# Kernel tuning notes

Measured on AMD Instinct MI355X. Metric: run time of the kernel, lower is better.

The kernel has to match this reference:

```python
import jax, jax.numpy as jnp
import numpy as np

H = 1024  # hidden_dim
DT = 0.1
LN_EPS = 1e-5


def setup_inputs() -> dict:
    key = jax.random.key(0)
    ks = jax.random.split(key, 8)
    h = H
    ph = h // 2
    x = jax.random.normal(ks[0], (8, 2048, h), dtype=jnp.float32)
    # S initialized to identity in torch; add small noise so math is non-trivial
    S = jnp.eye(h, dtype=jnp.float32) + 0.02 * jax.random.normal(ks[1], (h, h), dtype=jnp.float32)
    # Hamiltonian MLP: Linear(h,h) -> tanh -> Linear(h,1)
    lim1 = 1.0 / np.sqrt(h)
    W1 = jax.random.uniform(ks[2], (h, h), minval=-lim1, maxval=lim1, dtype=jnp.float32)
    b1 = jax.random.uniform(ks[3], (h,), minval=-lim1, maxval=lim1, dtype=jnp.float32)
    w2 = jax.random.uniform(ks[4], (h,), minval=-lim1, maxval=lim1, dtype=jnp.float32)
    b2 = jax.random.uniform(ks[5], (1,), minval=-lim1, maxval=lim1, dtype=jnp.float32)
    # symplectic structure matrix J (buffer)
    I = jnp.eye(ph, dtype=jnp.float32)
    J = jnp.zeros((h, h), dtype=jnp.float32)
    J = J.at[:ph, ph:].set(I)
    J = J.at[ph:, :ph].set(-I)
    gamma = jnp.ones((h,), dtype=jnp.float32)
    beta = jnp.zeros((h,), dtype=jnp.float32)
    return {"x": x, "S": S, "W1": W1, "b1": b1, "w2": w2, "b2": b2,
            "J": J, "gamma": gamma, "beta": beta, "num_steps": 3}


def reference(x, S, W1, b1, w2, b2, J, gamma, beta, num_steps):
    h = x.shape[-1]
    # Cayley-approx symplectic projection (training branch): S_sym = I + 2*A, A skew part
    A = (S - S.T) * 0.5
    S_sym = jnp.eye(h, dtype=x.dtype) + 2.0 * A
    # z = einsum('ij,...j->...i', S_sym, x)
    z = x @ S_sym.T
    for _ in range(num_steps):
        # analytic grad of H(z) = w2 . tanh(z W1^T + b1) + b2 wrt z
        t = jnp.tanh(z @ W1.T + b1)             # [..., h]
        grad_H = ((1.0 - t * t) * w2) @ W1       # [..., h]
        flow = grad_H @ J.T                      # einsum('ij,...j->...i', J, grad_H)
        z = z + DT * flow
    y = z + x
    # LayerNorm over last dim
    mu = jnp.mean(y, axis=-1, keepdims=True)
    var = jnp.mean((y - mu) ** 2, axis=-1, keepdims=True)
    return (y - mu) * jax.lax.rsqrt(var + LN_EPS) * gamma + beta
```

## Files before the change

kernel.cpp:

```cpp
#include <hip/hip_runtime.h>
#include <hip/hip_bf16.h>

#define H 1024
#define PH 512
#define MROWS 16384
#define DT 0.1f
#define LN_EPS 1e-5f

#define BM 128
#define BN 128
#define BK 64

typedef short s16x8 __attribute__((ext_vector_type(8)));
typedef float f32x4 __attribute__((ext_vector_type(4)));

__device__ __forceinline__ float b2f(short v) {
    union { float f; unsigned u; } c;
    c.u = ((unsigned)(unsigned short)v) << 16;
    return c.f;
}
__device__ __forceinline__ short f2b(float f) {
    union { float f; unsigned u; } c;
    c.f = f;
    unsigned u = c.u;
    unsigned r = u + 0x7FFFu + ((u >> 16) & 1u);
    return (short)(r >> 16);
}
__device__ __forceinline__ float ftanh(float s) {
    float e = __expf(2.0f * s);
    return 1.0f - 2.0f * __builtin_amdgcn_rcpf(e + 1.0f);
}

__global__ __launch_bounds__(256)
void prep_t(const float* __restrict__ S, const float* __restrict__ W1,
            short* __restrict__ Wsym, short* __restrict__ W1b,
            short* __restrict__ Wflow, short* __restrict__ WflowT) {
    __shared__ float T0[64][65];
    __shared__ float T1[64][65];
    __shared__ short Ts[64][66];
    const int I = blockIdx.y * 64, J = blockIdx.x * 64;
    const int c  = threadIdx.x & 63;
    const int r0 = (threadIdx.x >> 6) * 16;
#pragma unroll
    for (int rr = 0; rr < 16; ++rr) {
        int r = r0 + rr;
        T0[r][c] = S[(size_t)(I + r) * H + J + c];
        T1[r][c] = S[(size_t)(J + r) * H + I + c];
    }
    __syncthreads();
    const int pJ = (J + PH) & (H - 1);
    const short sflip = (J >= PH) ? (short)0x8000 : (short)0;
#pragma unroll
    for (int rr = 0; rr < 16; ++rr) {
        int r = r0 + rr;
        size_t rowb = (size_t)(I + r) * H;
        Wsym[rowb + J + c] = f2b(T0[r][c] - T1[c][r]);
        W1b [rowb + J + c] = f2b(W1[rowb + J + c]);
        short wt = (short)(f2b(W1[rowb + pJ + c]) ^ sflip);
        WflowT[rowb + J + c] = wt;
        Ts[r][c] = wt;
    }
    __syncthreads();
#pragma unroll
    for (int rr = 0; rr < 16; ++rr) {
        int r = r0 + rr;
        Wflow[(size_t)(J + r) * H + I + c] = Ts[c][r];
    }
}

__global__ __launch_bounds__(256)
void cvt_x(const float* __restrict__ x, short* __restrict__ xb) {
    int t = blockIdx.x * 256 + threadIdx.x;
    const float4* p = (const float4*)x + (size_t)t * 2;
    float4 f0 = p[0], f1 = p[1];
    s16x8 v;
    v[0] = f2b(f0.x); v[1] = f2b(f0.y); v[2] = f2b(f0.z); v[3] = f2b(f0.w);
    v[4] = f2b(f1.x); v[5] = f2b(f1.y); v[6] = f2b(f1.z); v[7] = f2b(f1.w);
    ((s16x8*)xb)[t] = v;
}

template <int KIND, bool G2D>
__global__ __launch_bounds__(256, 2)
void gemm_k(const short* __restrict__ A, const short* __restrict__ Bw,
            short* __restrict__ out,
            const float* __restrict__ xf,
            const float* __restrict__ w2f,
            const short* __restrict__ u0r,
            const short* __restrict__ pg,
            short* __restrict__ out2,
            float clampv)
{
    __shared__ short As[2][BM * BK];
    __shared__ short Bs[2][BN * BK];

    const int tid  = threadIdx.x;
    const int lane = tid & 63;
    const int wave = tid >> 6;
    const int wm   = wave >> 1;
    const int wn   = wave & 1;

    int m0, n0;
    if (G2D) {
        m0 = blockIdx.y * BM;
        n0 = blockIdx.x * BN;
    } else {
        const int lid   = blockIdx.x;
        const int chunk = ((lid & 7) << 7) | (lid >> 3);
        m0 = (chunk >> 3) * BM;
        n0 = (chunk & 7) * BN;
    }

    const int lrow = lane & 15;
    const int quad = lane >> 4;
    const int swzr = (lrow & 7) << 4;

    const int srow  = lane >> 3;
    const int selem = 8 * ((lane & 7) ^ srow);

    f32x4 acc[4][4] = {};

    auto STAGE = [&](int sel, int k0) {
#pragma unroll
        for (int i = 0; i < 4; ++i) {
            int ch = wave * 4 + i;
            const short* asrc = A  + (size_t)(m0 + ch * 8 + srow) * H + k0 + selem;
            const short* bsrc = Bw + (size_t)(n0 + ch * 8 + srow) * H + k0 + selem;
            __builtin_amdgcn_global_load_lds(
                (const __attribute__((address_space(1))) void*)asrc,
                (__attribute__((address_space(3))) void*)(&As[sel][ch * 512]), 16, 0, 0);
            __builtin_amdgcn_global_load_lds(
                (const __attribute__((address_space(1))) void*)bsrc,
                (__attribute__((address_space(3))) void*)(&Bs[sel][ch * 512]), 16, 0, 0);
        }
    };
    auto COMPUTE = [&](int sel) {
#pragma unroll
        for (int ks = 0; ks < 2; ++ks) {
            s16x8 af[4], bfr[4];
#pragma unroll
            for (int mt = 0; mt < 4; ++mt) {
                int row = wm * 64 + mt * 16 + lrow;
                af[mt] = *(const s16x8*)((const char*)&As[sel][0] + row * 128 +
                                         ((ks * 64 + quad * 16) ^ swzr));
            }
#pragma unroll
            for (int nt = 0; nt < 4; ++nt) {
                int col = wn * 64 + nt * 16 + lrow;
                bfr[nt] = *(const s16x8*)((const char*)&Bs[sel][0] + col * 128 +
                                          ((ks * 64 + quad * 16) ^ swzr));
            }
#pragma unroll
            for (int mt = 0; mt < 4; ++mt)
#pragma unroll
                for (int nt = 0; nt < 4; ++nt)
                    acc[mt][nt] = __builtin_amdgcn_mfma_f32_16x16x32_bf16(
                        bfr[nt], af[mt], acc[mt][nt], 0, 0, 0);
        }
    };

    STAGE(0, 0);
    int cur = 0;
    for (int t = 0; t < (H / BK) - 1; ++t) {
        STAGE(cur ^ 1, (t + 1) * BK);
        asm volatile("s_waitcnt vmcnt(8)" ::: "memory");
        __builtin_amdgcn_s_barrier();
        COMPUTE(cur);
        __builtin_amdgcn_s_barrier();
        cur ^= 1;
    }
    asm volatile("s_waitcnt vmcnt(0)" ::: "memory");
    __builtin_amdgcn_s_barrier();
    COMPUTE(cur);

    float4 bvv[4], wvv[4];
    if (KIND == 1 || KIND == 3 || KIND == 4) {
#pragma unroll
        for (int nt = 0; nt < 4; ++nt) {
            int col = n0 + wn * 64 + nt * 16 + quad * 4;
            bvv[nt] = *(const float4*)(xf + col);
            wvv[nt] = *(const float4*)(w2f + col);
        }
    }
#pragma unroll
    for (int mt = 0; mt < 4; ++mt) {
        const int row = m0 + wm * 64 + mt * 16 + lrow;
        const size_t rbase = (size_t)row * H;
#pragma unroll
        for (int nt = 0; nt < 4; ++nt) {
            const int col = n0 + wn * 64 + nt * 16 + quad * 4;
            const size_t idx = rbase + col;
            f32x4 a = acc[mt][nt];
            short4 o;
            if (KIND == 0) {
                float4 xv = *(const float4*)(xf + idx);
                o.x = f2b(a[0] + xv.x);
                o.y = f2b(a[1] + xv.y);
                o.z = f2b(a[2] + xv.z);
                o.w = f2b(a[3] + xv.w);
                *(short4*)(out + idx) = o;
            } else if (KIND == 1) {
                float t0 = ftanh(a[0] + bvv[nt].x);
                float t1 = ftanh(a[1] + bvv[nt].y);
                float t2 = ftanh(a[2] + bvv[nt].z);
                float t3 = ftanh(a[3] + bvv[nt].w);
                o.x = f2b((1.0f - t0 * t0) * wvv[nt].x);
                o.y = f2b((1.0f - t1 * t1) * wvv[nt].y);
                o.z = f2b((1.0f - t2 * t2) * wvv[nt].z);
                o.w = f2b((1.0f - t3 * t3) * wvv[nt].w);
                *(short4*)(out + idx) = o;
            } else if (KIND == 2) {
                short4 zo = *(const short4*)(out + idx);
                float d0 = fminf(fmaxf(DT * a[0], -clampv), clampv);
                float d1 = fminf(fmaxf(DT * a[1], -clampv), clampv);
                float d2 = fminf(fmaxf(DT * a[2], -clampv), clampv);
                float d3 = fminf(fmaxf(DT * a[3], -clampv), clampv);
                o.x = f2b(b2f(zo.x) + d0);
                o.y = f2b(b2f(zo.y) + d1);
                o.z = f2b(b2f(zo.z) + d2);
                o.w = f2b(b2f(zo.w) + d3);
                *(short4*)(out + idx) = o;
            } else if (KIND == 3) {
                short4 u;
                u.x = f2b(a[0]); u.y = f2b(a[1]); u.z = f2b(a[2]); u.w = f2b(a[3]);
                *(short4*)(out + idx) = u;
                float t0 = ftanh(a[0] + bvv[nt].x);
                float t1 = ftanh(a[1] + bvv[nt].y);
                float t2 = ftanh(a[2] + bvv[nt].z);
                float t3 = ftanh(a[3] + bvv[nt].w);
                o.x = f2b((1.0f - t0 * t0) * wvv[nt].x);
                o.y = f2b((1.0f - t1 * t1) * wvv[nt].y);
                o.z = f2b((1.0f - t2 * t2) * wvv[nt].z);
                o.w = f2b((1.0f - t3 * t3) * wvv[nt].w);
                *(short4*)(out2 + idx) = o;
            } else if (KIND == 4) {
                short4 u4 = *(const short4*)(u0r + idx);
                short4 p4 = *(const short4*)(pg + idx);
                float t0 = ftanh(b2f(u4.x) + a[0] + bvv[nt].x);
                float t1 = ftanh(b2f(u4.y) + a[1] + bvv[nt].y);
                float t2 = ftanh(b2f(u4.z) + a[2] + bvv[nt].z);
                float t3 = ftanh(b2f(u4.w) + a[3] + bvv[nt].w);
                o.x = f2b(b2f(p4.x) + (1.0f - t0 * t0) * wvv[nt].x);
                o.y = f2b(b2f(p4.y) + (1.0f - t1 * t1) * wvv[nt].y);
                o.z = f2b(b2f(p4.z) + (1.0f - t2 * t2) * wvv[nt].z);
                o.w = f2b(b2f(p4.w) + (1.0f - t3 * t3) * wvv[nt].w);
                *(short4*)(out2 + idx) = o;
            } else {
                o.x = f2b(DT * a[0]);
                o.y = f2b(DT * a[1]);
                o.z = f2b(DT * a[2]);
                o.w = f2b(DT * a[3]);
                *(short4*)(out + idx) = o;
            }
        }
    }
}

__global__ __launch_bounds__(256)
void ln_k(const short* __restrict__ z, const float* __restrict__ x,
          const float* __restrict__ gamma, const float* __restrict__ beta,
          float* __restrict__ out) {
    const int row = blockIdx.x;
    const int tid = threadIdx.x;
    const size_t base = (size_t)row * H;
    short4 z4 = ((const short4*)(z + base))[tid];
    float4 x4 = ((const float4*)(x + base))[tid];
    float y0 = b2f(z4.x) + x4.x;
    float y1 = b2f(z4.y) + x4.y;
    float y2 = b2f(z4.z) + x4.z;
    float y3 = b2f(z4.w) + x4.w;
    float s = y0 + y1 + y2 + y3;
    float q = y0 * y0 + y1 * y1 + y2 * y2 + y3 * y3;
#pragma unroll
    for (int off = 32; off > 0; off >>= 1) {
        s += __shfl_down(s, off);
        q += __shfl_down(q, off);
    }
    __shared__ float ss[4], qs[4];
    if ((tid & 63) == 0) { ss[tid >> 6] = s; qs[tid >> 6] = q; }
    __syncthreads();
    s = ss[0] + ss[1] + ss[2] + ss[3];
    q = qs[0] + qs[1] + qs[2] + qs[3];
    const float mu  = s * (1.0f / H);
    const float var = q * (1.0f / H) - mu * mu;
    const float rs  = rsqrtf(var + LN_EPS);
    const int col = tid * 4;
    float4 o;
    o.x = (y0 - mu) * rs * gamma[col + 0] + beta[col + 0];
    o.y = (y1 - mu) * rs * gamma[col + 1] + beta[col + 1];
    o.z = (y2 - mu) * rs * gamma[col + 2] + beta[col + 2];
    o.w = (y3 - mu) * rs * gamma[col + 3] + beta[col + 3];
    ((float4*)(out + base))[tid] = o;
}

extern "C" void kernel_launch(void* const* d_in, const int* in_sizes, int n_in,
                              void* d_out, int out_size, void* d_ws, size_t ws_size,
                              hipStream_t stream) {
    int ix = 0;
    for (int i = 0; i < n_in; ++i)
        if (in_sizes[i] == MROWS * H) { ix = i; break; }

    const float *x, *S, *W1, *b1, *w2, *gamma, *beta;
    if (ix == 0) {
        x     = (const float*)d_in[0];
        S     = (const float*)d_in[1];
        W1    = (const float*)d_in[2];
        b1    = (const float*)d_in[3];
        w2    = (const float*)d_in[4];
        gamma = (const float*)d_in[7];
        beta  = (const float*)d_in[8];
    } else {
        S     = (const float*)d_in[1];
        W1    = (const float*)d_in[2];
        b1    = (const float*)d_in[3];
        beta  = (const float*)d_in[5];
        gamma = (const float*)d_in[6];
        w2    = (const float*)d_in[8];
        x     = (const float*)d_in[ix];
    }

    const size_t MB = 1024 * 1024;
    float* out    = (float*)d_out;
    short* xb     = (short*)d_out;
    short* u0     = (short*)d_out;
    char*  hi     = (char*)d_out + 32 * MB;
    short* Wsym   = (short*)(hi);
    short* W1b    = (short*)(hi + 2 * MB);
    short* Wflow  = (short*)(hi + 4 * MB);
    short* WflowT = (short*)(hi + 6 * MB);
    short* GT     = (short*)(hi + 8 * MB);
    short* z      = (short*)d_ws;
    short* gsumA  = (short*)((char*)d_ws + 32 * MB);
    short* gsumB  = (short*)((char*)d_ws + 64 * MB);

    const bool fast = ws_size >= 96 * MB;

    prep_t<<<dim3(16, 16), 256, 0, stream>>>(S, W1, Wsym, W1b, Wflow, WflowT);
    cvt_x <<<(MROWS * H / 8) / 256, 256, 0, stream>>>(x, xb);

    const int nblk = (H / BN) * (MROWS / BM);
    if (fast) {
        gemm_k<5, true><<<dim3(H / BN, H / BM), 256, 0, stream>>>(
            W1b, WflowT, GT, nullptr, nullptr, nullptr, nullptr, nullptr, 0.0f);
        gemm_k<0, false><<<nblk, 256, 0, stream>>>(
            xb, Wsym, z, x, nullptr, nullptr, nullptr, nullptr, 0.0f);
        gemm_k<3, false><<<nblk, 256, 0, stream>>>(
            z, W1b, u0, b1, w2, nullptr, nullptr, gsumA, 0.0f);
        gemm_k<4, false><<<nblk, 256, 0, stream>>>(
            gsumA, GT, nullptr, b1, w2, u0, gsumA, gsumB, 0.0f);
        gemm_k<4, false><<<nblk, 256, 0, stream>>>(
            gsumB, GT, nullptr, b1, w2, u0, gsumB, gsumA, 0.0f);
        gemm_k<2, false><<<nblk, 256, 0, stream>>>(
            gsumA, Wflow, z, nullptr, nullptr, nullptr, nullptr, nullptr, 0.03f);
    } else {
        short* g = (short*)d_out;
        gemm_k<0, false><<<nblk, 256, 0, stream>>>(
            xb, Wsym, z, x, nullptr, nullptr, nullptr, nullptr, 0.0f);
        for (int step = 0; step < 3; ++step) {
            gemm_k<1, false><<<nblk, 256, 0, stream>>>(
                z, W1b, g, b1, w2, nullptr, nullptr, nullptr, 0.0f);
            gemm_k<2, false><<<nblk, 256, 0, stream>>>(
                g, Wflow, z, nullptr, nullptr, nullptr, nullptr, nullptr, 0.01f);
        }
    }
    ln_k<<<MROWS, 256, 0, stream>>>(z, x, gamma, beta, out);
}
```

Before: 426.6 us.

## Fold symmetric projection into weights, fuse final flow GEMM, single-buffer LDS

Precomputes Wu = W1·(S−Sᵀ)ᵀ-style combined weights so the first hidden GEMM reads bf16 x directly, which removes the separate z = x·S_symᵀ GEMM pass. It merges the final flow GEMM with the x·(S−Sᵀ) product into one GEMM with a doubled K (KIND 7). LayerNorm then adds 2x, which accounts for the identity part of S_sym. The GEMM drops LDS double buffering in favour of a single buffer with __syncthreads and raises the occupancy hint to 4 waves. The single buffer saves LDS for occupancy but loses load/compute overlap, and the reassociation changes bf16 rounding, including the dropped clamp on the fused path.

```diff
diff --git a/kernel.cpp b/kernel.cpp
--- a/kernel.cpp
+++ b/kernel.cpp
@@ -33,8 +33,9 @@
 
 __global__ __launch_bounds__(256)
 void prep_t(const float* __restrict__ S, const float* __restrict__ W1,
-            short* __restrict__ Wsym, short* __restrict__ W1b,
-            short* __restrict__ Wflow, short* __restrict__ WflowT) {
+            short* __restrict__ Wsym, short* __restrict__ WsymT,
+            short* __restrict__ W1b,
+            short* __restrict__ Wfd, short* __restrict__ WflowT) {
     __shared__ float T0[64][65];
     __shared__ float T1[64][65];
     __shared__ short Ts[64][66];
@@ -54,8 +55,10 @@
     for (int rr = 0; rr < 16; ++rr) {
         int r = r0 + rr;
         size_t rowb = (size_t)(I + r) * H;
-        Wsym[rowb + J + c] = f2b(T0[r][c] - T1[c][r]);
-        W1b [rowb + J + c] = f2b(W1[rowb + J + c]);
+        float d = T0[r][c] - T1[c][r];
+        Wsym [rowb + J + c] = f2b(d);
+        WsymT[rowb + J + c] = f2b(-d);
+        W1b  [rowb + J + c] = f2b(W1[rowb + J + c]);
         short wt = (short)(f2b(W1[rowb + pJ + c]) ^ sflip);
         WflowT[rowb + J + c] = wt;
         Ts[r][c] = wt;
@@ -64,7 +67,7 @@
 #pragma unroll
     for (int rr = 0; rr < 16; ++rr) {
         int r = r0 + rr;
-        Wflow[(size_t)(J + r) * H + I + c] = Ts[c][r];
+        Wfd[(size_t)(J + r) * H + I + c] = f2b(DT * b2f(Ts[c][r]));
     }
 }
 
@@ -80,7 +83,7 @@
 }
 
 template <int KIND, bool G2D>
-__global__ __launch_bounds__(256, 2)
+__global__ __launch_bounds__(256, 4)
 void gemm_k(const short* __restrict__ A, const short* __restrict__ Bw,
             short* __restrict__ out,
             const float* __restrict__ xf,
@@ -88,10 +91,12 @@
             const short* __restrict__ u0r,
             const short* __restrict__ pg,
             short* __restrict__ out2,
+            const short* __restrict__ A2,
+            const short* __restrict__ B2,
             float clampv)
 {
-    __shared__ short As[2][BM * BK];
-    __shared__ short Bs[2][BN * BK];
+    __shared__ short As[BM * BK];
+    __shared__ short Bs[BN * BK];
 
     const int tid  = threadIdx.x;
     const int lane = tid & 63;
@@ -119,34 +124,40 @@
 
     f32x4 acc[4][4] = {};
 
-    auto STAGE = [&](int sel, int k0) {
+    const int KSTEPS = (KIND == 7) ? (2 * H / BK) : (H / BK);
+    for (int t = 0; t < KSTEPS; ++t) {
+        const int k0 = t * BK;
+        const short* Au = A;
+        const short* Bu = Bw;
+        if (KIND == 7 && k0 >= H) { Au = A2; Bu = B2; }
+        const int kk = k0 & (H - 1);
 #pragma unroll
         for (int i = 0; i < 4; ++i) {
             int ch = wave * 4 + i;
-            const short* asrc = A  + (size_t)(m0 + ch * 8 + srow) * H + k0 + selem;
-            const short* bsrc = Bw + (size_t)(n0 + ch * 8 + srow) * H + k0 + selem;
+            const short* asrc = Au + (size_t)(m0 + ch * 8 + srow) * H + kk + selem;
+            const short* bsrc = Bu + (size_t)(n0 + ch * 8 + srow) * H + kk + selem;
             __builtin_amdgcn_global_load_lds(
                 (const __attribute__((address_space(1))) void*)asrc,
-                (__attribute__((address_space(3))) void*)(&As[sel][ch * 512]), 16, 0, 0);
+                (__attribute__((address_space(3))) void*)(As + ch * 512), 16, 0, 0);
             __builtin_amdgcn_global_load_lds(
                 (const __attribute__((address_space(1))) void*)bsrc,
-                (__attribute__((address_space(3))) void*)(&Bs[sel][ch * 512]), 16, 0, 0);
-        }
-    };
-    auto COMPUTE = [&](int sel) {
+                (__attribute__((address_space(3))) void*)(Bs + ch * 512), 16, 0, 0);
+        }
+        __syncthreads();
+
 #pragma unroll
         for (int ks = 0; ks < 2; ++ks) {
             s16x8 af[4], bfr[4];
 #pragma unroll
             for (int mt = 0; mt < 4; ++mt) {
                 int row = wm * 64 + mt * 16 + lrow;
-                af[mt] = *(const s16x8*)((const char*)&As[sel][0] + row * 128 +
+                af[mt] = *(const s16x8*)((const char*)As + row * 128 +
                                          ((ks * 64 + quad * 16) ^ swzr));
             }
 #pragma unroll
             for (int nt = 0; nt < 4; ++nt) {
                 int col = wn * 64 + nt * 16 + lrow;
-                bfr[nt] = *(const s16x8*)((const char*)&Bs[sel][0] + col * 128 +
+                bfr[nt] = *(const s16x8*)((const char*)Bs + col * 128 +
                                           ((ks * 64 + quad * 16) ^ swzr));
             }
 #pragma unroll
@@ -156,21 +167,8 @@
                     acc[mt][nt] = __builtin_amdgcn_mfma_f32_16x16x32_bf16(
                         bfr[nt], af[mt], acc[mt][nt], 0, 0, 0);
         }
-    };
-
-    STAGE(0, 0);
-    int cur = 0;
-    for (int t = 0; t < (H / BK) - 1; ++t) {
-        STAGE(cur ^ 1, (t + 1) * BK);
-        asm volatile("s_waitcnt vmcnt(8)" ::: "memory");
-        __builtin_amdgcn_s_barrier();
-        COMPUTE(cur);
-        __builtin_amdgcn_s_barrier();
-        cur ^= 1;
-    }
-    asm volatile("s_waitcnt vmcnt(0)" ::: "memory");
-    __builtin_amdgcn_s_barrier();
-    COMPUTE(cur);
+        __syncthreads();
+    }
 
     float4 bvv[4], wvv[4];
     if (KIND == 1 || KIND == 3 || KIND == 4) {
@@ -210,10 +208,10 @@
                 *(short4*)(out + idx) = o;
             } else if (KIND == 2) {
                 short4 zo = *(const short4*)(out + idx);
-                float d0 = fminf(fmaxf(DT * a[0], -clampv), clampv);
-                float d1 = fminf(fmaxf(DT * a[1], -clampv), clampv);
-                float d2 = fminf(fmaxf(DT * a[2], -clampv), clampv);
-                float d3 = fminf(fmaxf(DT * a[3], -clampv), clampv);
+                float d0 = fminf(fmaxf(a[0], -clampv), clampv);
+                float d1 = fminf(fmaxf(a[1], -clampv), clampv);
+                float d2 = fminf(fmaxf(a[2], -clampv), clampv);
+                float d3 = fminf(fmaxf(a[3], -clampv), clampv);
                 o.x = f2b(b2f(zo.x) + d0);
                 o.y = f2b(b2f(zo.y) + d1);
                 o.z = f2b(b2f(zo.z) + d2);
@@ -244,12 +242,18 @@
                 o.z = f2b(b2f(p4.z) + (1.0f - t2 * t2) * wvv[nt].z);
                 o.w = f2b(b2f(p4.w) + (1.0f - t3 * t3) * wvv[nt].w);
                 *(short4*)(out2 + idx) = o;
-            } else {
+            } else if (KIND == 5) {
                 o.x = f2b(DT * a[0]);
                 o.y = f2b(DT * a[1]);
                 o.z = f2b(DT * a[2]);
                 o.w = f2b(DT * a[3]);
                 *(short4*)(out + idx) = o;
+            } else {
+                o.x = f2b(a[0]);
+                o.y = f2b(a[1]);
+                o.z = f2b(a[2]);
+                o.w = f2b(a[3]);
+                *(short4*)(out + idx) = o;
             }
         }
     }
@@ -258,16 +262,16 @@
 __global__ __launch_bounds__(256)
 void ln_k(const short* __restrict__ z, const float* __restrict__ x,
           const float* __restrict__ gamma, const float* __restrict__ beta,
-          float* __restrict__ out) {
+          float* __restrict__ out, float xmul) {
     const int row = blockIdx.x;
     const int tid = threadIdx.x;
     const size_t base = (size_t)row * H;
     short4 z4 = ((const short4*)(z + base))[tid];
     float4 x4 = ((const float4*)(x + base))[tid];
-    float y0 = b2f(z4.x) + x4.x;
-    float y1 = b2f(z4.y) + x4.y;
-    float y2 = b2f(z4.z) + x4.z;
-    float y3 = b2f(z4.w) + x4.w;
+    float y0 = fmaf(xmul, x4.x, b2f(z4.x));
+    float y1 = fmaf(xmul, x4.y, b2f(z4.y));
+    float y2 = fmaf(xmul, x4.z, b2f(z4.z));
+    float y3 = fmaf(xmul, x4.w, b2f(z4.w));
     float s = y0 + y1 + y2 + y3;
     float q = y0 * y0 + y1 * y1 + y2 * y2 + y3 * y3;
 #pragma unroll
@@ -320,47 +324,62 @@
 
     const size_t MB = 1024 * 1024;
     float* out    = (float*)d_out;
-    short* xb     = (short*)d_out;
     short* u0     = (short*)d_out;
     char*  hi     = (char*)d_out + 32 * MB;
     short* Wsym   = (short*)(hi);
-    short* W1b    = (short*)(hi + 2 * MB);
-    short* Wflow  = (short*)(hi + 4 * MB);
+    short* WsymT  = (short*)(hi + 2 * MB);
+    short* W1b    = (short*)(hi + 4 * MB);
     short* WflowT = (short*)(hi + 6 * MB);
-    short* GT     = (short*)(hi + 8 * MB);
-    short* z      = (short*)d_ws;
+    short* Wfd    = (short*)(hi + 8 * MB);
+    short* Wu     = (short*)(hi + 10 * MB);
+    short* GT     = (short*)(hi + 12 * MB);
+    short* xb     = (short*)d_ws;
     short* gsumA  = (short*)((char*)d_ws + 32 * MB);
     short* gsumB  = (short*)((char*)d_ws + 64 * MB);
+    short* z      = gsumB;
 
     const bool fast = ws_size >= 96 * MB;
-
-    prep_t<<<dim3(16, 16), 256, 0, stream>>>(S, W1, Wsym, W1b, Wflow, WflowT);
-    cvt_x <<<(MROWS * H / 8) / 256, 256, 0, stream>>>(x, xb);
-
-    const int nblk = (H / BN) * (MROWS / BM);
+    const int  nblk = (H / BN) * (MROWS / BM);
+
+    prep_t<<<dim3(16, 16), 256, 0, stream>>>(S, W1, Wsym, WsymT, W1b, Wfd, WflowT);
+
     if (fast) {
+        cvt_x<<<(MROWS * H / 8) / 256, 256, 0, stream>>>(x, xb);
+        gemm_k<0, true><<<dim3(H / BN, H / BM), 256, 0, stream>>>(
+            W1b, WsymT, Wu, W1, nullptr, nullptr, nullptr, nullptr,
+            nullptr, nullptr, 0.0f);
         gemm_k<5, true><<<dim3(H / BN, H / BM), 256, 0, stream>>>(
-            W1b, WflowT, GT, nullptr, nullptr, nullptr, nullptr, nullptr, 0.0f);
+            W1b, WflowT, GT, nullptr, nullptr, nullptr, nullptr, nullptr,
+            nullptr, nullptr, 0.0f);
+        gemm_k<3, false><<<nblk, 256, 0, stream>>>(
+            xb, Wu, u0, b1, w2, nullptr, nullptr, gsumA,
+            nullptr, nullptr, 0.0f);
+        gemm_k<4, false><<<nblk, 256, 0, stream>>>(
+            gsumA, GT, nullptr, b1, w2, u0, gsumA, gsumB,
+            nullptr, nullptr, 0.0f);
+        gemm_k<4, false><<<nblk, 256, 0, stream>>>(
+            gsumB, GT, nullptr, b1, w2, u0, gsumB, gsumA,
+            nullptr, nullptr, 0.0f);
+        gemm_k<7, false><<<nblk, 256, 0, stream>>>(
+            xb, Wsym, z, nullptr, nullptr, nullptr, nullptr, nullptr,
+            gsumA, Wfd, 0.0f);
+        ln_k<<<MROWS, 256, 0, stream>>>(z, x, gamma, beta, out, 2.0f);
+    } else {
+        short* xbo = (short*)d_out;
+        short* go  = (short*)d_out;
+        short* zf  = (short*)d_ws;
+        cvt_x<<<(MROWS * H / 8) / 256, 256, 0, stream>>>(x, xbo);
         gemm_k<0, false><<<nblk, 256, 0, stream>>>(
-            xb, Wsym, z, x, nullptr, nullptr, nullptr, nullptr, 0.0f);
-        gemm_k<3, false><<<nblk, 256, 0, stream>>>(
-            z, W1b, u0, b1, w2, nullptr, nullptr, gsumA, 0.0f);
-        gemm_k<4, false><<<nblk, 256, 0, stream>>>(
-            gsumA, GT, nullptr, b1, w2, u0, gsumA, gsumB, 0.0f);
-        gemm_k<4, false><<<nblk, 256, 0, stream>>>(
-            gsumB, GT, nullptr, b1, w2, u0, gsumB, gsumA, 0.0f);
-        gemm_k<2, false><<<nblk, 256, 0, stream>>>(
-            gsumA, Wflow, z, nullptr, nullptr, nullptr, nullptr, nullptr, 0.03f);
-    } else {
-        short* g = (short*)d_out;
-        gemm_k<0, false><<<nblk, 256, 0, stream>>>(
-            xb, Wsym, z, x, nullptr, nullptr, nullptr, nullptr, 0.0f);
+            xbo, Wsym, zf, x, nullptr, nullptr, nullptr, nullptr,
+            nullptr, nullptr, 0.0f);
         for (int step = 0; step < 3; ++step) {
             gemm_k<1, false><<<nblk, 256, 0, stream>>>(
-                z, W1b, g, b1, w2, nullptr, nullptr, nullptr, 0.0f);
+                zf, W1b, go, b1, w2, nullptr, nullptr, nullptr,
+                nullptr, nullptr, 0.0f);
             gemm_k<2, false><<<nblk, 256, 0, stream>>>(
-                g, Wflow, z, nullptr, nullptr, nullptr, nullptr, nullptr, 0.01f);
-        }
-    }
-    ln_k<<<MROWS, 256, 0, stream>>>(z, x, gamma, beta, out);
-}
+                go, Wfd, zf, nullptr, nullptr, nullptr, nullptr, nullptr,
+                nullptr, nullptr, 0.01f);
+        }
+        ln_k<<<MROWS, 256, 0, stream>>>(zf, x, gamma, beta, out, 1.0f);
+    }
+}
```

Measured after the change: 415.6 us. -2.6%, faster.
